# Kernel tuning notes

Hardware: AMD Instinct MI355X
Metric: run time of the kernel (lower is better)

Reference implementation:

```python
import jax, jax.numpy as jnp
import numpy as np

COL = 14
NJ = 23
SIGMA = 1.0
RADIUS = int(4.0 * SIGMA + 0.5)  # scipy gaussian_filter default truncate=4.0


def _gauss_matrix(col=COL, sigma=SIGMA, radius=RADIUS):
    """col x col matrix M such that (M @ img @ M.T) == scipy gaussian_filter(img, sigma)
    with scipy's default 'reflect' boundary (== numpy 'symmetric')."""
    xs = np.arange(-radius, radius + 1)
    w = np.exp(-0.5 * (xs / sigma) ** 2)
    w = (w / w.sum()).astype(np.float32)
    M = np.zeros((col, col), np.float32)
    for out in range(col):
        for k in range(-radius, radius + 1):
            i = (out + k) % (2 * col)
            if i >= col:
                i = 2 * col - 1 - i
            M[out, i] += w[k + radius]
    return M

_M = jnp.asarray(_gauss_matrix())


def setup_inputs() -> dict:
    key = jax.random.key(0)
    k0, k1, k2, k3 = jax.random.split(key, 4)
    B = 4096
    o = jax.random.normal(k0, (B, 3 * NJ, COL, COL), dtype=jnp.float32)
    h = jax.random.uniform(k1, (B, NJ, COL, COL), dtype=jnp.float32)
    t = jax.random.uniform(k2, (B, NJ, 3), dtype=jnp.float32)
    v = jax.random.randint(k3, (B, NJ, 2), 0, 2, dtype=jnp.int32)
    return {"o": o, "h": h, "t": t, "v": v}


def reference(o, h, t, v):
    B = h.shape[0]
    scale = 1.0 / COL

    # per-joint argmax over the heatmap -> integer (y, x) coords
    idx = jnp.argmax(h.reshape(B, NJ, COL * COL), axis=-1)  # [B, Nj]
    y = idx // COL
    x = idx % COL

    bi = jnp.arange(B)[:, None]
    ji = jnp.arange(NJ)[None, :]
    px = o[bi, ji, y, x] + x.astype(h.dtype) * scale
    py = o[bi, ji + NJ, y, x] + y.astype(h.dtype) * scale
    pz = o[bi, ji + 2 * NJ, y, x]
    pred = jnp.stack([px, py, pz], axis=-1)  # [B, Nj, 3]

    # target heatmaps: delta at (yi, xi), gaussian-filtered, min-max normalized
    ti = t * COL
    xi = jnp.trunc(ti[..., 0]).astype(jnp.int32)  # int() truncation as in torch code
    yi = jnp.trunc(ti[..., 1]).astype(jnp.int32)
    in_range = (xi >= 0) & (xi <= COL - 1) & (yi >= 0) & (yi <= COL - 1)
    mask = (v[..., 0] == 1) & in_range  # [B, Nj]

    xc = jnp.clip(xi, 0, COL - 1)
    yc = jnp.clip(yi, 0, COL - 1)
    # gaussian_filter of a one-hot delta is the outer product of two filter columns
    gy = _M.T[yc]  # [B, Nj, COL], gy[..., r] = M[r, yc]
    gx = _M.T[xc]  # [B, Nj, COL]
    tt_map = gy[..., :, None] * gx[..., None, :]  # [B, Nj, COL, COL]
    mn = tt_map.min(axis=(-2, -1), keepdims=True)
    mx = tt_map.max(axis=(-2, -1), keepdims=True)
    tt = (tt_map - mn) / (mx - mn)
    tt = tt * mask[..., None, None].astype(h.dtype)

    d1 = jnp.sum((h - tt) ** 2) / NJ
    d2 = jnp.sum((pred - t) ** 2) / NJ
    return d1 + d2
```

## Files before the change

### kernel.cpp

```cpp
#include <hip/hip_runtime.h>
#include <math.h>

#define COL 14
#define NJ 23
#define BATCH 4096
#define NJOINT (BATCH * NJ)
#define RADIUS 4
#define THREADS 256
#define BLOCKS 2048
#define WAVES_TOTAL (BLOCKS * (THREADS / 64))

__global__ __launch_bounds__(THREADS) void msq3d_kernel(
    const float* __restrict__ o,
    const float* __restrict__ h,
    const float* __restrict__ t,
    const int*   __restrict__ v,
    float* __restrict__ out)
{
    __shared__ float sM[COL * COL];
    __shared__ float sColMin[COL], sColMax[COL];
    __shared__ float sWaveSum[THREADS / 64];

    const int tid = threadIdx.x;

    if (tid < COL * COL) {
        double wd[2 * RADIUS + 1];
        double wsum = 0.0;
        #pragma unroll
        for (int k = 0; k <= 2 * RADIUS; ++k) {
            double xx = (double)(k - RADIUS);
            wd[k] = exp(-0.5 * xx * xx);
            wsum += wd[k];
        }
        const int outr = tid / COL, ic = tid % COL;
        float acc = 0.0f;
        #pragma unroll
        for (int k = -RADIUS; k <= RADIUS; ++k) {
            int ii = (outr + k) % (2 * COL);
            if (ii < 0) ii += 2 * COL;
            if (ii >= COL) ii = 2 * COL - 1 - ii;
            if (ii == ic) acc += (float)(wd[k + RADIUS] / wsum);
        }
        sM[outr * COL + ic] = acc;
    }
    __syncthreads();
    if (tid < COL) {
        float mn = sM[tid], mx = mn;
        for (int r = 1; r < COL; ++r) {
            float x = sM[r * COL + tid];
            mn = fminf(mn, x);
            mx = fmaxf(mx, x);
        }
        sColMin[tid] = mn;
        sColMax[tid] = mx;
    }
    __syncthreads();

    const int lane = tid & 63;
    const int wave_in_blk = tid >> 6;
    const int gwave = blockIdx.x * (THREADS / 64) + wave_in_blk;
    const float scale = 1.0f / (float)COL;

    const bool act = (lane < 49);
    const int q0 = lane * 4;
    int rk[4], ck[4];
    #pragma unroll
    for (int k = 0; k < 4; ++k) {
        int q = q0 + k;
        if (q > COL * COL - 1) q = COL * COL - 1;
        rk[k] = q / COL;
        ck[k] = q - rk[k] * COL;
    }

    float accD = 0.0f;

    for (int joint = gwave; joint < NJOINT; joint += WAVES_TOTAL) {
        const int b = joint / NJ;
        const int j = joint - b * NJ;

        const float t0 = t[joint * 3 + 0];
        const float t1 = t[joint * 3 + 1];
        const float t2 = t[joint * 3 + 2];
        const int   v0 = v[joint * 2 + 0];

        const int xi = (int)truncf(t0 * (float)COL);
        const int yi = (int)truncf(t1 * (float)COL);
        const bool in_range = (xi >= 0) && (xi <= COL - 1) && (yi >= 0) && (yi <= COL - 1);
        const bool mask = (v0 == 1) && in_range;
        const int xc = min(max(xi, 0), COL - 1);
        const int yc = min(max(yi, 0), COL - 1);

        const float4* hb4 = (const float4*)(h + (size_t)joint * (COL * COL));
        float4 hv4 = make_float4(0.f, 0.f, 0.f, 0.f);
        if (act) hv4 = hb4[lane];
        const float hv[4] = {hv4.x, hv4.y, hv4.z, hv4.w};

        float lv = -INFINITY;
        int   lq = 0;
        if (act) {
            #pragma unroll
            for (int k = 0; k < 4; ++k) {
                if (hv[k] > lv) { lv = hv[k]; lq = q0 + k; }
            }
        }

        if (mask) {
            const float mn  = sColMin[yc] * sColMin[xc];
            const float mx  = sColMax[yc] * sColMax[xc];
            const float inv = 1.0f / (mx - mn);
            if (act) {
                #pragma unroll
                for (int k = 0; k < 4; ++k) {
                    float ttv = (sM[rk[k] * COL + yc] * sM[ck[k] * COL + xc] - mn) * inv;
                    float d = hv[k] - ttv;
                    accD += d * d;
                }
            }
        } else if (act) {
            #pragma unroll
            for (int k = 0; k < 4; ++k)
                accD += hv[k] * hv[k];
        }

        float wmax = lv;
        #pragma unroll
        for (int off = 1; off < 64; off <<= 1)
            wmax = fmaxf(wmax, __shfl_xor(wmax, off, 64));
        unsigned long long mb = __ballot(act && (lv == wmax));
        const int src = (int)(__ffsll((long long)mb) - 1);
        const int besti = __shfl(lq, src, 64);

        if (lane == 0) {
            const int y = besti / COL;
            const int x = besti - y * COL;
            const size_t ob = (((size_t)b * (3 * NJ) + j) * COL + y) * COL + x;
            const float o0 = o[ob];
            const float o1 = o[ob + (size_t)NJ * COL * COL];
            const float o2 = o[ob + (size_t)(2 * NJ) * COL * COL];
            const float dx = (o0 + (float)x * scale) - t0;
            const float dy = (o1 + (float)y * scale) - t1;
            const float dz = o2 - t2;
            accD += dx * dx + dy * dy + dz * dz;
        }
    }

    #pragma unroll
    for (int off = 32; off > 0; off >>= 1)
        accD += __shfl_down(accD, off, 64);
    if (lane == 0) sWaveSum[wave_in_blk] = accD;
    __syncthreads();
    if (tid == 0) {
        float s = 0.0f;
        #pragma unroll
        for (int w = 0; w < THREADS / 64; ++w) s += sWaveSum[w];
        atomicAdd(out, s * (1.0f / (float)NJ));
    }
}

extern "C" void kernel_launch(void* const* d_in, const int* in_sizes, int n_in,
                              void* d_out, int out_size, void* d_ws, size_t ws_size,
                              hipStream_t stream) {
    const float* o = (const float*)d_in[0];
    const float* h = (const float*)d_in[1];
    const float* t = (const float*)d_in[2];
    const int*   v = (const int*)d_in[3];
    float* out = (float*)d_out;

    hipMemsetAsync(d_out, 0, sizeof(float), stream);
    msq3d_kernel<<<BLOCKS, THREADS, 0, stream>>>(o, h, t, v, out);
}
```

Before: 327.5 us.

## Prefetch next joint's heatmap and targets; split o gathers across three lanes

Software-pipelines the per-wave joint loop so the next joint's heatmap row, target and visibility loads are issued before the current joint is processed, hiding global-memory latency. The three o gathers are spread across lanes 0-2 instead of serialized on lane 0. Block count is reduced so waves iterate more times, which gives the prefetch something to overlap. The cost is higher register pressure from the double-buffered values. The first-iteration load assumes every wave has at least one joint, which holds for this grid size.

```diff
diff --git a/kernel.cpp b/kernel.cpp
--- a/kernel.cpp
+++ b/kernel.cpp
@@ -7,7 +7,7 @@
 #define NJOINT (BATCH * NJ)
 #define RADIUS 4
 #define THREADS 256
-#define BLOCKS 2048
+#define BLOCKS 1472
 #define WAVES_TOTAL (BLOCKS * (THREADS / 64))
 
 __global__ __launch_bounds__(THREADS) void msq3d_kernel(
@@ -74,14 +74,34 @@
 
     float accD = 0.0f;
 
-    for (int joint = gwave; joint < NJOINT; joint += WAVES_TOTAL) {
+    int joint = gwave;
+    float4 hv4 = make_float4(0.f, 0.f, 0.f, 0.f);
+    {
+        const float4* hb4 = (const float4*)(h + (size_t)joint * (COL * COL));
+        if (act) hv4 = hb4[lane];
+    }
+    float t0 = t[joint * 3 + 0];
+    float t1 = t[joint * 3 + 1];
+    float t2 = t[joint * 3 + 2];
+    int   v0 = v[joint * 2 + 0];
+
+    for (;;) {
+        const int jn = joint + WAVES_TOTAL;
+        const bool more = (jn < NJOINT);
+        float4 nh4 = make_float4(0.f, 0.f, 0.f, 0.f);
+        float nt0 = 0.f, nt1 = 0.f, nt2 = 0.f;
+        int   nv0 = 0;
+        if (more) {
+            const float4* nb4 = (const float4*)(h + (size_t)jn * (COL * COL));
+            if (act) nh4 = nb4[lane];
+            nt0 = t[jn * 3 + 0];
+            nt1 = t[jn * 3 + 1];
+            nt2 = t[jn * 3 + 2];
+            nv0 = v[jn * 2 + 0];
+        }
+
         const int b = joint / NJ;
         const int j = joint - b * NJ;
-
-        const float t0 = t[joint * 3 + 0];
-        const float t1 = t[joint * 3 + 1];
-        const float t2 = t[joint * 3 + 2];
-        const int   v0 = v[joint * 2 + 0];
 
         const int xi = (int)truncf(t0 * (float)COL);
         const int yi = (int)truncf(t1 * (float)COL);
@@ -90,9 +110,6 @@
         const int xc = min(max(xi, 0), COL - 1);
         const int yc = min(max(yi, 0), COL - 1);
 
-        const float4* hb4 = (const float4*)(h + (size_t)joint * (COL * COL));
-        float4 hv4 = make_float4(0.f, 0.f, 0.f, 0.f);
-        if (act) hv4 = hb4[lane];
         const float hv[4] = {hv4.x, hv4.y, hv4.z, hv4.w};
 
         float lv = -INFINITY;
@@ -130,18 +147,22 @@
         const int src = (int)(__ffsll((long long)mb) - 1);
         const int besti = __shfl(lq, src, 64);
 
-        if (lane == 0) {
-            const int y = besti / COL;
-            const int x = besti - y * COL;
-            const size_t ob = (((size_t)b * (3 * NJ) + j) * COL + y) * COL + x;
-            const float o0 = o[ob];
-            const float o1 = o[ob + (size_t)NJ * COL * COL];
-            const float o2 = o[ob + (size_t)(2 * NJ) * COL * COL];
-            const float dx = (o0 + (float)x * scale) - t0;
-            const float dy = (o1 + (float)y * scale) - t1;
-            const float dz = o2 - t2;
-            accD += dx * dx + dy * dy + dz * dz;
+        const int by = besti / COL;
+        const int bx = besti - by * COL;
+        if (lane < 3) {
+            const size_t ob = (((size_t)b * (3 * NJ) + j + lane * NJ) * COL + by) * COL + bx;
+            const float ov = o[ob];
+            const float addv = (lane == 0) ? (float)bx * scale
+                             : (lane == 1) ? (float)by * scale : 0.0f;
+            const float tc = (lane == 0) ? t0 : (lane == 1) ? t1 : t2;
+            const float d = (ov + addv) - tc;
+            accD += d * d;
         }
+
+        if (!more) break;
+        joint = jn;
+        hv4 = nh4;
+        t0 = nt0; t1 = nt1; t2 = nt2; v0 = nv0;
     }
 
     #pragma unroll
```

Measured after the change: 320.8 us. 1.02x faster.

## Process two joints per wave with software-prefetched loads and deferred gather

Applied to the files above, without the earlier changes.

Restructures the per-wave loop to handle two joints per iteration and prefetch the next pair's heatmap, target and visibility data one iteration ahead. The o gather is spread over three lanes, and its squared error is accumulated one iteration later so the load latency overlaps other work. The grid is resized so each wave gets an exact trip count of joints. This raises register pressure and hard-codes the problem size into the loop bounds.

```diff
diff --git a/kernel.cpp b/kernel.cpp
--- a/kernel.cpp
+++ b/kernel.cpp
@@ -7,8 +7,10 @@
 #define NJOINT (BATCH * NJ)
 #define RADIUS 4
 #define THREADS 256
-#define BLOCKS 2048
+#define BLOCKS 1472
 #define WAVES_TOTAL (BLOCKS * (THREADS / 64))
+#define JPW (NJOINT / WAVES_TOTAL)
+#define PAIRS (JPW / 2)
 
 __global__ __launch_bounds__(THREADS) void msq3d_kernel(
     const float* __restrict__ o,
@@ -60,6 +62,7 @@
     const int wave_in_blk = tid >> 6;
     const int gwave = blockIdx.x * (THREADS / 64) + wave_in_blk;
     const float scale = 1.0f / (float)COL;
+    const int W = WAVES_TOTAL;
 
     const bool act = (lane < 49);
     const int q0 = lane * 4;
@@ -74,74 +77,146 @@
 
     float accD = 0.0f;
 
-    for (int joint = gwave; joint < NJOINT; joint += WAVES_TOTAL) {
-        const int b = joint / NJ;
-        const int j = joint - b * NJ;
-
-        const float t0 = t[joint * 3 + 0];
-        const float t1 = t[joint * 3 + 1];
-        const float t2 = t[joint * 3 + 2];
-        const int   v0 = v[joint * 2 + 0];
-
-        const int xi = (int)truncf(t0 * (float)COL);
-        const int yi = (int)truncf(t1 * (float)COL);
-        const bool in_range = (xi >= 0) && (xi <= COL - 1) && (yi >= 0) && (yi <= COL - 1);
-        const bool mask = (v0 == 1) && in_range;
-        const int xc = min(max(xi, 0), COL - 1);
-        const int yc = min(max(yi, 0), COL - 1);
-
-        const float4* hb4 = (const float4*)(h + (size_t)joint * (COL * COL));
-        float4 hv4 = make_float4(0.f, 0.f, 0.f, 0.f);
-        if (act) hv4 = hb4[lane];
-        const float hv[4] = {hv4.x, hv4.y, hv4.z, hv4.w};
-
-        float lv = -INFINITY;
-        int   lq = 0;
+    int jA = gwave;
+    int jB = gwave + W;
+    float4 hA = make_float4(0.f, 0.f, 0.f, 0.f);
+    float4 hB = make_float4(0.f, 0.f, 0.f, 0.f);
+    if (act) {
+        hA = ((const float4*)(h + (size_t)jA * (COL * COL)))[lane];
+        hB = ((const float4*)(h + (size_t)jB * (COL * COL)))[lane];
+    }
+    float tA0 = t[jA * 3 + 0], tA1 = t[jA * 3 + 1], tA2 = t[jA * 3 + 2];
+    float tB0 = t[jB * 3 + 0], tB1 = t[jB * 3 + 1], tB2 = t[jB * 3 + 2];
+    int   vA0 = v[jA * 2 + 0];
+    int   vB0 = v[jB * 2 + 0];
+
+    float povA = 0.f, pcA = 0.f, povB = 0.f, pcB = 0.f;
+
+    #pragma unroll 1
+    for (int p = 0; p < PAIRS; ++p) {
+        float4 nA = make_float4(0.f, 0.f, 0.f, 0.f);
+        float4 nB = make_float4(0.f, 0.f, 0.f, 0.f);
+        float ntA0 = 0.f, ntA1 = 0.f, ntA2 = 0.f;
+        float ntB0 = 0.f, ntB1 = 0.f, ntB2 = 0.f;
+        int   nvA0 = 0, nvB0 = 0;
+        if (p + 1 < PAIRS) {
+            const int njA = jA + 2 * W;
+            const int njB = jB + 2 * W;
+            if (act) {
+                nA = ((const float4*)(h + (size_t)njA * (COL * COL)))[lane];
+                nB = ((const float4*)(h + (size_t)njB * (COL * COL)))[lane];
+            }
+            ntA0 = t[njA * 3 + 0]; ntA1 = t[njA * 3 + 1]; ntA2 = t[njA * 3 + 2];
+            ntB0 = t[njB * 3 + 0]; ntB1 = t[njB * 3 + 1]; ntB2 = t[njB * 3 + 2];
+            nvA0 = v[njA * 2 + 0];
+            nvB0 = v[njB * 2 + 0];
+        }
+
+        const int bA = jA / NJ, jjA = jA - bA * NJ;
+        const int bB = jB / NJ, jjB = jB - bB * NJ;
+
+        const int xiA = (int)truncf(tA0 * (float)COL);
+        const int yiA = (int)truncf(tA1 * (float)COL);
+        const int xiB = (int)truncf(tB0 * (float)COL);
+        const int yiB = (int)truncf(tB1 * (float)COL);
+        const bool maskA = (vA0 == 1) && (xiA >= 0) && (xiA <= COL - 1) && (yiA >= 0) && (yiA <= COL - 1);
+        const bool maskB = (vB0 == 1) && (xiB >= 0) && (xiB <= COL - 1) && (yiB >= 0) && (yiB <= COL - 1);
+        const int xcA = min(max(xiA, 0), COL - 1), ycA = min(max(yiA, 0), COL - 1);
+        const int xcB = min(max(xiB, 0), COL - 1), ycB = min(max(yiB, 0), COL - 1);
+
+        const float hvA[4] = {hA.x, hA.y, hA.z, hA.w};
+        const float hvB[4] = {hB.x, hB.y, hB.z, hB.w};
+
+        float lvA = -INFINITY, lvB = -INFINITY;
+        int   lqA = 0, lqB = 0;
         if (act) {
             #pragma unroll
             for (int k = 0; k < 4; ++k) {
-                if (hv[k] > lv) { lv = hv[k]; lq = q0 + k; }
-            }
-        }
-
-        if (mask) {
-            const float mn  = sColMin[yc] * sColMin[xc];
-            const float mx  = sColMax[yc] * sColMax[xc];
+                if (hvA[k] > lvA) { lvA = hvA[k]; lqA = q0 + k; }
+                if (hvB[k] > lvB) { lvB = hvB[k]; lqB = q0 + k; }
+            }
+        }
+
+        if (maskA) {
+            const float mn  = sColMin[ycA] * sColMin[xcA];
+            const float mx  = sColMax[ycA] * sColMax[xcA];
             const float inv = 1.0f / (mx - mn);
             if (act) {
                 #pragma unroll
                 for (int k = 0; k < 4; ++k) {
-                    float ttv = (sM[rk[k] * COL + yc] * sM[ck[k] * COL + xc] - mn) * inv;
-                    float d = hv[k] - ttv;
+                    float ttv = (sM[rk[k] * COL + ycA] * sM[ck[k] * COL + xcA] - mn) * inv;
+                    float d = hvA[k] - ttv;
                     accD += d * d;
                 }
             }
         } else if (act) {
             #pragma unroll
             for (int k = 0; k < 4; ++k)
-                accD += hv[k] * hv[k];
-        }
-
-        float wmax = lv;
-        #pragma unroll
-        for (int off = 1; off < 64; off <<= 1)
-            wmax = fmaxf(wmax, __shfl_xor(wmax, off, 64));
-        unsigned long long mb = __ballot(act && (lv == wmax));
-        const int src = (int)(__ffsll((long long)mb) - 1);
-        const int besti = __shfl(lq, src, 64);
-
-        if (lane == 0) {
-            const int y = besti / COL;
-            const int x = besti - y * COL;
-            const size_t ob = (((size_t)b * (3 * NJ) + j) * COL + y) * COL + x;
-            const float o0 = o[ob];
-            const float o1 = o[ob + (size_t)NJ * COL * COL];
-            const float o2 = o[ob + (size_t)(2 * NJ) * COL * COL];
-            const float dx = (o0 + (float)x * scale) - t0;
-            const float dy = (o1 + (float)y * scale) - t1;
-            const float dz = o2 - t2;
-            accD += dx * dx + dy * dy + dz * dz;
-        }
+                accD += hvA[k] * hvA[k];
+        }
+        if (maskB) {
+            const float mn  = sColMin[ycB] * sColMin[xcB];
+            const float mx  = sColMax[ycB] * sColMax[xcB];
+            const float inv = 1.0f / (mx - mn);
+            if (act) {
+                #pragma unroll
+                for (int k = 0; k < 4; ++k) {
+                    float ttv = (sM[rk[k] * COL + ycB] * sM[ck[k] * COL + xcB] - mn) * inv;
+                    float d = hvB[k] - ttv;
+                    accD += d * d;
+                }
+            }
+        } else if (act) {
+            #pragma unroll
+            for (int k = 0; k < 4; ++k)
+                accD += hvB[k] * hvB[k];
+        }
+
+        float wA = lvA, wB = lvB;
+        #pragma unroll
+        for (int off = 1; off < 64; off <<= 1) {
+            wA = fmaxf(wA, __shfl_xor(wA, off, 64));
+            wB = fmaxf(wB, __shfl_xor(wB, off, 64));
+        }
+        unsigned long long mbA = __ballot(act && (lvA == wA));
+        unsigned long long mbB = __ballot(act && (lvB == wB));
+        const int srcA = (int)(__ffsll((long long)mbA) - 1);
+        const int srcB = (int)(__ffsll((long long)mbB) - 1);
+        const int bestiA = __shfl(lqA, srcA, 64);
+        const int bestiB = __shfl(lqB, srcB, 64);
+
+        if (lane < 3) {
+            const float dA = povA + pcA;
+            const float dB = povB + pcB;
+            accD += dA * dA + dB * dB;
+        }
+
+        const int byA = bestiA / COL, bxA = bestiA - (bestiA / COL) * COL;
+        const int byB = bestiB / COL, bxB = bestiB - (bestiB / COL) * COL;
+        if (lane < 3) {
+            const size_t obA = (((size_t)bA * (3 * NJ) + jjA + lane * NJ) * COL + byA) * COL + bxA;
+            const size_t obB = (((size_t)bB * (3 * NJ) + jjB + lane * NJ) * COL + byB) * COL + bxB;
+            povA = o[obA];
+            povB = o[obB];
+            pcA = (lane == 0) ? ((float)bxA * scale - tA0)
+                : (lane == 1) ? ((float)byA * scale - tA1)
+                : (-tA2);
+            pcB = (lane == 0) ? ((float)bxB * scale - tB0)
+                : (lane == 1) ? ((float)byB * scale - tB1)
+                : (-tB2);
+        }
+
+        jA += 2 * W; jB += 2 * W;
+        hA = nA; hB = nB;
+        tA0 = ntA0; tA1 = ntA1; tA2 = ntA2;
+        tB0 = ntB0; tB1 = ntB1; tB2 = ntB2;
+        vA0 = nvA0; vB0 = nvB0;
+    }
+
+    if (lane < 3) {
+        const float dA = povA + pcA;
+        const float dB = povB + pcB;
+        accD += dA * dA + dB * dB;
     }
 
     #pragma unroll
```

After: 325.6 us. Within noise of the previous version (-0.6%).
